# Optimization experiments

Measured on AMD Instinct MI355X. Metric: run time of the kernel, lower is better.

## Reference

```python
import jax, jax.numpy as jnp
import numpy as np

EPS = 1e-12          # F.normalize eps
TEMP = 10.0          # softmax temperature scale
SCENE_THRESHOLD = 0.8
MEMORY_SIZE = 512
MEMORY_DIM = 256
BATCH = 131072


def _l2_normalize(x, axis):
    # matches torch F.normalize: x / max(||x||_2, eps)
    n = jnp.linalg.norm(x, axis=axis, keepdims=True)
    return x / jnp.maximum(n, EPS)


def setup_inputs() -> dict:
    key = jax.random.key(0)
    kq, kk, kv = jax.random.split(key, 3)
    query = jax.random.normal(kq, (BATCH, MEMORY_DIM), dtype=jnp.float32)
    # kaiming-uniform-ish init for the memory bank
    bound = float(np.sqrt(6.0 / MEMORY_DIM))
    memory_keys = jax.random.uniform(kk, (MEMORY_SIZE, MEMORY_DIM), dtype=jnp.float32, minval=-bound, maxval=bound)
    memory_values = jax.random.uniform(kv, (MEMORY_SIZE, MEMORY_DIM), dtype=jnp.float32, minval=-bound, maxval=bound)
    return {"query": query, "memory_keys": memory_keys, "memory_values": memory_values}


def reference(query, memory_keys, memory_values):
    query_norm = _l2_normalize(query, axis=1)          # [B, D]
    memory_norm = _l2_normalize(memory_keys, axis=1)   # [M, D]
    similarity = jnp.einsum('bd,md->bm', query_norm, memory_norm)  # [B, M]
    weights = jax.nn.softmax(similarity * TEMP, axis=1)            # [B, M]
    output = jnp.einsum('bm,md->bd', weights, memory_values)       # [B, D]
    # scene change detection (batch_size > 1 path)
    scene_diff = jnp.linalg.norm(query[1:] - query[:-1], axis=1)   # [B-1]
    same_scene = scene_diff < SCENE_THRESHOLD
    return output, weights, same_scene
```

## Files before the change

kernel.cpp:

```cpp
#include <hip/hip_runtime.h>
#include <hip/hip_bf16.h>

#define DIM 256
#define MEMN 512
#define TEMPF 10.0f

typedef float f32x4 __attribute__((ext_vector_type(4)));
typedef __bf16 bf16x8 __attribute__((ext_vector_type(8)));
typedef unsigned int u32;
typedef unsigned short u16;

__device__ __forceinline__ u16 bf16bits(float x) {
  __bf16 h = (__bf16)x;
  return __builtin_bit_cast(u16, h);
}
__device__ __forceinline__ u32 pack2(float a, float b) {
  return (u32)bf16bits(a) | ((u32)bf16bits(b) << 16);
}

__global__ void prep_keys(const float* __restrict__ keys, u16* __restrict__ knf) {
  int lane = threadIdx.x & 63;
  int m = blockIdx.x * 4 + (threadIdx.x >> 6);
  float4 v = *reinterpret_cast<const float4*>(keys + (size_t)m * DIM + lane * 4);
  float ss = v.x*v.x + v.y*v.y + v.z*v.z + v.w*v.w;
  #pragma unroll
  for (int o = 1; o < 64; o <<= 1) ss += __shfl_xor(ss, o);
  float rn = 1.0f / fmaxf(sqrtf(ss), 1e-12f);
  float vals[4] = {v.x*rn, v.y*rn, v.z*rn, v.w*rn};
  int mt = m >> 4, ml = m & 15;
  #pragma unroll
  for (int t = 0; t < 4; ++t) {
    int d = lane * 4 + t;
    int kc = d >> 5, gg = (d >> 3) & 3, j = d & 7;
    knf[(size_t)((kc*32 + mt)*64 + gg*16 + ml)*8 + j] = bf16bits(vals[t]);
  }
}

__global__ void prep_vals(const float* __restrict__ mv, u16* __restrict__ vtf) {
  int lane = threadIdx.x & 63;
  int m = blockIdx.x * 4 + (threadIdx.x >> 6);
  float4 v = *reinterpret_cast<const float4*>(mv + (size_t)m * DIM + lane * 4);
  float vals[4] = {v.x, v.y, v.z, v.w};
  int kc = m >> 5, gg = (m >> 3) & 3, j = m & 7;
  #pragma unroll
  for (int t = 0; t < 4; ++t) {
    int d = lane * 4 + t;
    int dt = d >> 4, dl = d & 15;
    vtf[(size_t)((kc*16 + dt)*64 + gg*16 + dl)*8 + j] = bf16bits(vals[t]);
  }
}

#define BAR_LGKM do { \
    asm volatile("s_waitcnt lgkmcnt(0)" ::: "memory"); \
    __builtin_amdgcn_s_barrier(); \
  } while (0)

__global__ __launch_bounds__(256, 2) void fused_main(
    const float* __restrict__ q, const u16* __restrict__ knf,
    const u16* __restrict__ vtf, float* __restrict__ out_o,
    float* __restrict__ out_w, float* __restrict__ out_s) {
  __shared__ __align__(16) char lds[66816];
  const int tid = threadIdx.x;
  const int wave = tid >> 6, lane = tid & 63;
  const int g = lane >> 4, c = lane & 15;
  const int browbase = blockIdx.x * 64;
  const int myrow = browbase + wave * 16 + c;

  float* psb = reinterpret_cast<float*>(lds + 65536);
  float* rnb = reinterpret_cast<float*>(lds + 66560);

  const float* qrow = q + (size_t)myrow * DIM + g * 8;
  float sd = 0.f, ss = 0.f;
  #pragma unroll
  for (int kc = 0; kc < 8; ++kc) {
    f32x4 a = __builtin_nontemporal_load(reinterpret_cast<const f32x4*>(qrow + kc*32));
    f32x4 b = __builtin_nontemporal_load(reinterpret_cast<const f32x4*>(qrow + kc*32 + 4));
    float x[8] = {a[0], a[1], a[2], a[3], b[0], b[1], b[2], b[3]};
    bf16x8 qb;
    #pragma unroll
    for (int e = 0; e < 8; ++e) {
      float nb = __shfl_down(x[e], 1);
      float d0 = nb - x[e];
      sd += d0 * d0;
      ss += x[e] * x[e];
      qb[e] = (__bf16)x[e];
    }
    *reinterpret_cast<bf16x8*>(lds + (wave*8 + kc)*1024 + lane*16) = qb;
  }
  sd += __shfl_xor(sd, 16); sd += __shfl_xor(sd, 32);
  ss += __shfl_xor(ss, 16); ss += __shfl_xor(ss, 32);
  if (g == 0 && c < 15)
    out_s[myrow] = (sqrtf(sd) < 0.8f) ? 1.0f : 0.0f;
  float rn = 1.0f / fmaxf(sqrtf(ss), 1e-12f);
  if (g == 0) rnb[wave*16 + c] = rn;
  BAR_LGKM;

  float scale_r[4];
  #pragma unroll
  for (int gr = 0; gr < 4; ++gr) scale_r[gr] = TEMPF * rnb[gr*16 + c];

  f32x4 acc[8][4];
  #pragma unroll
  for (int mt = 0; mt < 8; ++mt)
    #pragma unroll
    for (int gr = 0; gr < 4; ++gr) { f32x4 z = {}; acc[mt][gr] = z; }

  #pragma unroll
  for (int kc = 0; kc < 8; ++kc) {
    bf16x8 bfr[4];
    #pragma unroll
    for (int gr = 0; gr < 4; ++gr)
      bfr[gr] = *reinterpret_cast<const bf16x8*>(lds + (gr*8 + kc)*1024 + lane*16);
    bf16x8 afr[8];
    #pragma unroll
    for (int mt = 0; mt < 8; ++mt)
      afr[mt] = *reinterpret_cast<const bf16x8*>(
          knf + (size_t)(kc*32 + wave*8 + mt)*512 + lane*8);
    #pragma unroll
    for (int mt = 0; mt < 8; ++mt)
      #pragma unroll
      for (int gr = 0; gr < 4; ++gr)
        acc[mt][gr] = __builtin_amdgcn_mfma_f32_16x16x32_bf16(afr[mt], bfr[gr], acc[mt][gr], 0, 0, 0);
  }

  float psum[4] = {0.f, 0.f, 0.f, 0.f};
  #pragma unroll
  for (int mt = 0; mt < 8; ++mt)
    #pragma unroll
    for (int gr = 0; gr < 4; ++gr)
      #pragma unroll
      for (int i = 0; i < 4; ++i) {
        float e = __expf(acc[mt][gr][i] * scale_r[gr]);
        acc[mt][gr][i] = e;
        psum[gr] += e;
      }
  #pragma unroll
  for (int gr = 0; gr < 4; ++gr) {
    psum[gr] += __shfl_xor(psum[gr], 16);
    psum[gr] += __shfl_xor(psum[gr], 32);
  }
  if (g == 0) {
    #pragma unroll
    for (int gr = 0; gr < 4; ++gr)
      psb[(wave*4 + gr)*16 + c] = psum[gr];
  }
  BAR_LGKM;

  float rcp_r[4];
  #pragma unroll
  for (int gr = 0; gr < 4; ++gr) {
    float t = psb[(0*4 + gr)*16 + c] + psb[(1*4 + gr)*16 + c]
            + psb[(2*4 + gr)*16 + c] + psb[(3*4 + gr)*16 + c];
    rcp_r[gr] = 1.0f / t;
  }
  #pragma unroll
  for (int mt = 0; mt < 8; ++mt)
    #pragma unroll
    for (int gr = 0; gr < 4; ++gr)
      #pragma unroll
      for (int i = 0; i < 4; ++i)
        acc[mt][gr][i] *= rcp_r[gr];

  #pragma unroll
  for (int mt = 0; mt < 8; ++mt) {
    int kcw = 4*wave + (mt >> 1);
    int lane_t = ((mt & 1)*2 + (g >> 1))*16 + c;
    #pragma unroll
    for (int gr = 0; gr < 4; ++gr) {
      u32 lo = pack2(acc[mt][gr][0], acc[mt][gr][1]);
      u32 hi = pack2(acc[mt][gr][2], acc[mt][gr][3]);
      u32* dst = reinterpret_cast<u32*>(lds + (size_t)(kcw*4 + gr)*1024 + lane_t*16 + (g & 1)*8);
      dst[0] = lo; dst[1] = hi;
    }
  }
  BAR_LGKM;

  f32x4 oacc[4][4];
  #pragma unroll
  for (int dt = 0; dt < 4; ++dt)
    #pragma unroll
    for (int gr = 0; gr < 4; ++gr) { f32x4 z = {}; oacc[dt][gr] = z; }

  #pragma unroll
  for (int kc2 = 0; kc2 < 16; ++kc2) {
    bf16x8 bfr[4];
    #pragma unroll
    for (int gr = 0; gr < 4; ++gr)
      bfr[gr] = *reinterpret_cast<const bf16x8*>(lds + (size_t)(kc2*4 + gr)*1024 + lane*16);
    bf16x8 afr[4];
    #pragma unroll
    for (int dt = 0; dt < 4; ++dt)
      afr[dt] = *reinterpret_cast<const bf16x8*>(
          vtf + (size_t)(kc2*16 + wave*4 + dt)*512 + lane*8);
    #pragma unroll
    for (int dt = 0; dt < 4; ++dt)
      #pragma unroll
      for (int gr = 0; gr < 4; ++gr)
        oacc[dt][gr] = __builtin_amdgcn_mfma_f32_16x16x32_bf16(afr[dt], bfr[gr], oacc[dt][gr], 0, 0, 0);
  }
  BAR_LGKM;

  char* priv = lds + wave * 16384;

  #pragma unroll
  for (int dt = 0; dt < 4; ++dt)
    #pragma unroll
    for (int gr = 0; gr < 4; ++gr) {
      int row = gr*16 + c;
      *reinterpret_cast<f32x4*>(priv + row*256 + ((dt*64 + g*16) ^ (c << 4))) = oacc[dt][gr];
    }
  #pragma unroll
  for (int p = 0; p < 16; ++p) {
    int rq = lane >> 4, cc = lane & 15;
    int rowp = 4*p + rq;
    f32x4 t = *reinterpret_cast<const f32x4*>(priv + rowp*256 + ((cc*16) ^ ((rowp & 15) << 4)));
    __builtin_nontemporal_store(t, reinterpret_cast<f32x4*>(
        out_o + (size_t)(browbase + rowp)*DIM + wave*64 + cc*4));
  }

  #pragma unroll
  for (int h = 0; h < 2; ++h) {
    #pragma unroll
    for (int mt = 0; mt < 8; ++mt)
      #pragma unroll
      for (int grl = 0; grl < 2; ++grl) {
        int row = grl*16 + c;
        *reinterpret_cast<f32x4*>(priv + row*512 + ((mt*64 + g*16) ^ (c << 4))) = acc[mt][2*h + grl];
      }
    #pragma unroll
    for (int p = 0; p < 16; ++p) {
      int rq = lane >> 5, cc = lane & 31;
      int rowp = 2*p + rq;
      f32x4 t = *reinterpret_cast<const f32x4*>(priv + rowp*512 + ((cc*16) ^ ((rowp & 15) << 4)));
      __builtin_nontemporal_store(t, reinterpret_cast<f32x4*>(
          out_w + (size_t)(browbase + h*32 + rowp)*MEMN + wave*128 + cc*4));
    }
  }
}

__global__ void scene_bound(const float* __restrict__ q, float* __restrict__ out_s, int B) {
  int widx = (blockIdx.x * blockDim.x + threadIdx.x) >> 6;
  int lane = threadIdx.x & 63;
  int i = widx * 16 + 15;
  if (i > B - 2) return;
  const float* a = q + (size_t)i * DIM + lane * 4;
  float4 x = *reinterpret_cast<const float4*>(a);
  float4 y = *reinterpret_cast<const float4*>(a + DIM);
  float dx = y.x-x.x, dy = y.y-x.y, dz = y.z-x.z, dw = y.w-x.w;
  float sd = dx*dx + dy*dy + dz*dz + dw*dw;
  #pragma unroll
  for (int o = 1; o < 64; o <<= 1) sd += __shfl_xor(sd, o);
  if (lane == 0) out_s[i] = (sqrtf(sd) < 0.8f) ? 1.0f : 0.0f;
}

extern "C" void kernel_launch(void* const* d_in, const int* in_sizes, int n_in,
                              void* d_out, int out_size, void* d_ws, size_t ws_size,
                              hipStream_t stream) {
  const float* q  = (const float*)d_in[0];
  const float* mk = (const float*)d_in[1];
  const float* mv = (const float*)d_in[2];
  int B = in_sizes[0] / DIM;
  float* o = (float*)d_out;
  float* w = o + (size_t)B * DIM;
  float* s = w + (size_t)B * MEMN;
  u16* knf = (u16*)d_ws;
  u16* vtf = (u16*)((char*)d_ws + 262144);
  prep_keys<<<128, 256, 0, stream>>>(mk, knf);
  prep_vals<<<128, 256, 0, stream>>>(mv, vtf);
  fused_main<<<B / 64, 256, 0, stream>>>(q, knf, vtf, o, w, s);
  int nwaves = B / 16;
  scene_bound<<<(nwaves + 3) / 4, 256, 0, stream>>>(q, s, B);
}
```

Before: 153.8 us.

## Halve LDS footprint to raise occupancy by splitting PV stage into two halves

```diff
diff --git a/kernel.cpp b/kernel.cpp
--- a/kernel.cpp
+++ b/kernel.cpp
@@ -55,19 +55,19 @@
     __builtin_amdgcn_s_barrier(); \
   } while (0)
 
-__global__ __launch_bounds__(256, 2) void fused_main(
+__global__ __launch_bounds__(256, 4) void fused_main(
     const float* __restrict__ q, const u16* __restrict__ knf,
     const u16* __restrict__ vtf, float* __restrict__ out_o,
     float* __restrict__ out_w, float* __restrict__ out_s) {
-  __shared__ __align__(16) char lds[66816];
+  __shared__ __align__(16) char lds[34048];
   const int tid = threadIdx.x;
   const int wave = tid >> 6, lane = tid & 63;
   const int g = lane >> 4, c = lane & 15;
   const int browbase = blockIdx.x * 64;
   const int myrow = browbase + wave * 16 + c;
 
-  float* psb = reinterpret_cast<float*>(lds + 65536);
-  float* rnb = reinterpret_cast<float*>(lds + 66560);
+  float* psb = reinterpret_cast<float*>(lds + 32768);
+  float* rnb = reinterpret_cast<float*>(lds + 33792);
 
   const float* qrow = q + (size_t)myrow * DIM + g * 8;
   float sd = 0.f, ss = 0.f;
@@ -161,19 +161,19 @@
       for (int i = 0; i < 4; ++i)
         acc[mt][gr][i] *= rcp_r[gr];
 
-  #pragma unroll
-  for (int mt = 0; mt < 8; ++mt) {
-    int kcw = 4*wave + (mt >> 1);
-    int lane_t = ((mt & 1)*2 + (g >> 1))*16 + c;
-    #pragma unroll
-    for (int gr = 0; gr < 4; ++gr) {
-      u32 lo = pack2(acc[mt][gr][0], acc[mt][gr][1]);
-      u32 hi = pack2(acc[mt][gr][2], acc[mt][gr][3]);
-      u32* dst = reinterpret_cast<u32*>(lds + (size_t)(kcw*4 + gr)*1024 + lane_t*16 + (g & 1)*8);
-      dst[0] = lo; dst[1] = hi;
-    }
-  }
-  BAR_LGKM;
+#define WFRAG_WRITE(SLOTBASE) \
+    _Pragma("unroll") \
+    for (int mt = 0; mt < 8; ++mt) { \
+      int slot = (4*wave + (mt >> 1) - (SLOTBASE)) * 4; \
+      int lane_t = ((mt & 1)*2 + (g >> 1))*16 + c; \
+      _Pragma("unroll") \
+      for (int gr = 0; gr < 4; ++gr) { \
+        u32 lo = pack2(acc[mt][gr][0], acc[mt][gr][1]); \
+        u32 hi = pack2(acc[mt][gr][2], acc[mt][gr][3]); \
+        u32* dst = reinterpret_cast<u32*>(lds + (size_t)(slot + gr)*1024 + lane_t*16 + (g & 1)*8); \
+        dst[0] = lo; dst[1] = hi; \
+      } \
+    }
 
   f32x4 oacc[4][4];
   #pragma unroll
@@ -181,8 +181,11 @@
     #pragma unroll
     for (int gr = 0; gr < 4; ++gr) { f32x4 z = {}; oacc[dt][gr] = z; }
 
-  #pragma unroll
-  for (int kc2 = 0; kc2 < 16; ++kc2) {
+  if (wave < 2) { WFRAG_WRITE(0) }
+  BAR_LGKM;
+
+  #pragma unroll
+  for (int kc2 = 0; kc2 < 8; ++kc2) {
     bf16x8 bfr[4];
     #pragma unroll
     for (int gr = 0; gr < 4; ++gr)
@@ -200,40 +203,61 @@
   }
   BAR_LGKM;
 
-  char* priv = lds + wave * 16384;
-
-  #pragma unroll
-  for (int dt = 0; dt < 4; ++dt)
-    #pragma unroll
-    for (int gr = 0; gr < 4; ++gr) {
-      int row = gr*16 + c;
-      *reinterpret_cast<f32x4*>(priv + row*256 + ((dt*64 + g*16) ^ (c << 4))) = oacc[dt][gr];
-    }
-  #pragma unroll
-  for (int p = 0; p < 16; ++p) {
-    int rq = lane >> 4, cc = lane & 15;
-    int rowp = 4*p + rq;
-    f32x4 t = *reinterpret_cast<const f32x4*>(priv + rowp*256 + ((cc*16) ^ ((rowp & 15) << 4)));
-    __builtin_nontemporal_store(t, reinterpret_cast<f32x4*>(
-        out_o + (size_t)(browbase + rowp)*DIM + wave*64 + cc*4));
-  }
-
-  #pragma unroll
-  for (int h = 0; h < 2; ++h) {
+  if (wave >= 2) { WFRAG_WRITE(8) }
+  BAR_LGKM;
+
+  #pragma unroll
+  for (int kc2 = 8; kc2 < 16; ++kc2) {
+    bf16x8 bfr[4];
+    #pragma unroll
+    for (int gr = 0; gr < 4; ++gr)
+      bfr[gr] = *reinterpret_cast<const bf16x8*>(lds + (size_t)((kc2-8)*4 + gr)*1024 + lane*16);
+    bf16x8 afr[4];
+    #pragma unroll
+    for (int dt = 0; dt < 4; ++dt)
+      afr[dt] = *reinterpret_cast<const bf16x8*>(
+          vtf + (size_t)(kc2*16 + wave*4 + dt)*512 + lane*8);
+    #pragma unroll
+    for (int dt = 0; dt < 4; ++dt)
+      #pragma unroll
+      for (int gr = 0; gr < 4; ++gr)
+        oacc[dt][gr] = __builtin_amdgcn_mfma_f32_16x16x32_bf16(afr[dt], bfr[gr], oacc[dt][gr], 0, 0, 0);
+  }
+  BAR_LGKM;
+
+  char* priv = lds + wave * 8192;
+
+  #pragma unroll
+  for (int ho = 0; ho < 2; ++ho) {
+    #pragma unroll
+    for (int dt = 0; dt < 4; ++dt)
+      #pragma unroll
+      for (int grl = 0; grl < 2; ++grl) {
+        int rowl = grl*16 + c;
+        *reinterpret_cast<f32x4*>(priv + rowl*256 + ((dt*64 + g*16) ^ (c << 4))) = oacc[dt][ho*2 + grl];
+      }
+    #pragma unroll
+    for (int p = 0; p < 8; ++p) {
+      int rq = lane >> 4, cc = lane & 15;
+      int rowp = 4*p + rq;
+      f32x4 t = *reinterpret_cast<const f32x4*>(priv + rowp*256 + ((cc*16) ^ ((rowp & 15) << 4)));
+      __builtin_nontemporal_store(t, reinterpret_cast<f32x4*>(
+          out_o + (size_t)(browbase + ho*32 + rowp)*DIM + wave*64 + cc*4));
+    }
+  }
+
+  #pragma unroll
+  for (int gw = 0; gw < 4; ++gw) {
     #pragma unroll
     for (int mt = 0; mt < 8; ++mt)
-      #pragma unroll
-      for (int grl = 0; grl < 2; ++grl) {
-        int row = grl*16 + c;
-        *reinterpret_cast<f32x4*>(priv + row*512 + ((mt*64 + g*16) ^ (c << 4))) = acc[mt][2*h + grl];
-      }
-    #pragma unroll
-    for (int p = 0; p < 16; ++p) {
+      *reinterpret_cast<f32x4*>(priv + c*512 + ((mt*64 + g*16) ^ (c << 4))) = acc[mt][gw];
+    #pragma unroll
+    for (int p = 0; p < 8; ++p) {
       int rq = lane >> 5, cc = lane & 31;
       int rowp = 2*p + rq;
       f32x4 t = *reinterpret_cast<const f32x4*>(priv + rowp*512 + ((cc*16) ^ ((rowp & 15) << 4)));
       __builtin_nontemporal_store(t, reinterpret_cast<f32x4*>(
-          out_w + (size_t)(browbase + h*32 + rowp)*MEMN + wave*128 + cc*4));
+          out_w + (size_t)(browbase + gw*16 + rowp)*MEMN + wave*128 + cc*4));
     }
   }
 }
```

Result: slower. 535.0 us (+247.8%).
